# Kernel tuning notes

Hardware: AMD Instinct MI355X
Metric: run time of the kernel (lower is better)

## Reference

```python
import jax, jax.numpy as jnp
import numpy as np

GRID_SIZE = 5
SPLINE_ORDER = 3
NUM_BASIS = GRID_SIZE + SPLINE_ORDER  # 8

def _grid():
    # Extended knot vector over [-1, 1]: G + 2k + 1 knots
    h = 2.0 / GRID_SIZE
    return jnp.asarray(-1.0 + h * np.arange(-SPLINE_ORDER, GRID_SIZE + SPLINE_ORDER + 1), dtype=jnp.float32)

def _bspline_basis(x, grid, k):
    # x: [B, D] -> bases [B, D, G + k] via Cox-de Boor recursion
    xe = x[..., None]
    b = ((xe >= grid[:-1]) & (xe < grid[1:])).astype(x.dtype)
    for p in range(1, k + 1):
        left = (xe - grid[:-(p + 1)]) / (grid[p:-1] - grid[:-(p + 1)]) * b[..., :-1]
        right = (grid[p + 1:] - xe) / (grid[p + 1:] - grid[1:-p]) * b[..., 1:]
        b = left + right
    return b

def setup_inputs() -> dict:
    key = jax.random.key(0)
    ks = jax.random.split(key, 10)
    B, D, U = 2048, 1024, 1024
    L = 3  # number of KAN sub-layers
    s = 0.05
    return {
        "x": jax.random.normal(ks[0], (B, D), jnp.float32),
        "h_prev": jax.random.normal(ks[1], (B, U), jnp.float32),
        "c_prev": jax.random.normal(ks[2], (B, U), jnp.float32),
        "lstm_kernel": jax.random.normal(ks[3], (D, 4 * U), jnp.float32) * s,
        "lstm_rkernel": jax.random.normal(ks[4], (U, 4 * U), jnp.float32) * s,
        "lstm_bias": jnp.zeros((4 * U,), jnp.float32),
        "kan_base_w": jax.random.normal(ks[5], (L, D, U), jnp.float32) * s,
        "kan_spline_w": jax.random.normal(ks[6], (L, D * NUM_BASIS, U), jnp.float32) * s,
        "combine_w": jax.random.normal(ks[7], (U + L * U, U), jnp.float32) * s,
        "combine_b": jnp.zeros((U,), jnp.float32),
    }

def reference(x, h_prev, c_prev, lstm_kernel, lstm_rkernel, lstm_bias,
              kan_base_w, kan_spline_w, combine_w, combine_b):
    B, D = x.shape
    L, _, U = kan_base_w.shape
    # --- LSTM cell (Keras gate order i, f, g, o) ---
    z = x @ lstm_kernel + h_prev @ lstm_rkernel + lstm_bias
    zi, zf, zg, zo = jnp.split(z, 4, axis=-1)
    c = jax.nn.sigmoid(zf) * c_prev + jax.nn.sigmoid(zi) * jnp.tanh(zg)
    h = jax.nn.sigmoid(zo) * jnp.tanh(c)
    lstm_out = h
    # --- KAN sub-layers: silu(x) @ W_base + Bspline(x) @ W_spline ---
    grid = _grid()
    bases = _bspline_basis(x, grid, SPLINE_ORDER)           # [B, D, K]
    base_out = jnp.einsum('bd,ldu->lbu', jax.nn.silu(x), kan_base_w)
    spline_w = kan_spline_w.reshape(L, D, NUM_BASIS, U)
    spline_out = jnp.einsum('bdk,ldku->lbu', bases, spline_w)
    kan_out = base_out + spline_out                          # [L, B, U]
    kan_concat = jnp.transpose(kan_out, (1, 0, 2)).reshape(B, L * U)
    # --- fuse ---
    combined = jnp.concatenate([lstm_out, kan_concat], axis=-1)
    output = combined @ combine_w + combine_b
    return (output, h, c)
```

## Files before the change

kernel.cpp:

```cpp
#include <hip/hip_runtime.h>
#include <hip/hip_bf16.h>
#include <math.h>

#define B_SZ 2048
#define D_SZ 1024
#define U_SZ 1024
#define L_SZ 3
#define NB 8
#define KAN_K (D_SZ + D_SZ * NB)
#define KAN_N (L_SZ * U_SZ)
#define LSTM_K (D_SZ + U_SZ)
#define COMB_K (U_SZ + L_SZ * U_SZ)
#define LSTM_N (4 * U_SZ)

typedef __attribute__((ext_vector_type(8))) short bhalf8_t;
typedef __attribute__((ext_vector_type(4))) float floatx4_t;

__device__ inline void async_copy16(const void* g, void* l) {
  __builtin_amdgcn_global_load_lds(
      (const __attribute__((address_space(1))) void*)g,
      (__attribute__((address_space(3))) void*)l, 16, 0, 0);
}

__device__ inline float fsig(float v) { return 1.f / (1.f + __expf(-v)); }
__device__ inline float ftanh(float v) { return 1.f - 2.f / (__expf(2.f * v) + 1.f); }
__device__ inline unsigned short bfb(float v) {
  __hip_bfloat16 h = __float2bfloat16(v);
  return *(unsigned short*)&h;
}

__global__ __launch_bounds__(256) void prep_trans(
    const float* __restrict__ x, const float* __restrict__ h_prev,
    const float* __restrict__ lstm_k, const float* __restrict__ lstm_r,
    const float* __restrict__ comb_w, const float* __restrict__ base_w,
    const float* __restrict__ spline_w,
    __hip_bfloat16* __restrict__ A1, __hip_bfloat16* __restrict__ Akan,
    __hip_bfloat16* __restrict__ Bt1, __hip_bfloat16* __restrict__ Btc,
    __hip_bfloat16* __restrict__ Btk) {
  __shared__ float tile[64][65];
  int bid = blockIdx.x;
  int tid = threadIdx.x;
  if (bid < 8192) {
    int idx = bid * 256 + tid;
    int b = idx >> 10, d = idx & 1023;
    float xv = x[idx];
    float hv = h_prev[idx];
    A1[(size_t)b * LSTM_K + d] = __float2bfloat16(xv);
    A1[(size_t)b * LSTM_K + D_SZ + d] = __float2bfloat16(hv);
    float sg = 1.0f / (1.0f + __expf(-xv));
    Akan[(size_t)b * KAN_K + d] = __float2bfloat16(xv * sg);
    float t[12];
#pragma unroll
    for (int i = 0; i < 12; ++i) t[i] = (float)(-1.0 + 0.4 * (double)(i - 3));
    float bb[11];
#pragma unroll
    for (int j = 0; j < 11; ++j) bb[j] = (xv >= t[j] && xv < t[j + 1]) ? 1.0f : 0.0f;
#pragma unroll
    for (int p = 1; p <= 3; ++p) {
#pragma unroll
      for (int j = 0; j + p < 11; ++j) {
        float invl = 1.0f / (t[j + p] - t[j]);
        float invr = 1.0f / (t[j + p + 1] - t[j + 1]);
        bb[j] = (xv - t[j]) * invl * bb[j] + (t[j + p + 1] - xv) * invr * bb[j + 1];
      }
    }
    unsigned short o[8];
#pragma unroll
    for (int j = 0; j < 8; ++j) o[j] = bfb(bb[j]);
    *(uint4*)(Akan + (size_t)b * KAN_K + D_SZ + d * 8) = *(uint4*)o;
    return;
  }
  int id = bid - 8192;
  const float* src;
  __hip_bfloat16* dst;
  int srcLd, dstLd, gxs;
  if (id < 1024) {
    src = lstm_k; dst = Bt1; srcLd = 4096; dstLd = 2048; gxs = 6;
  } else if (id < 2048) {
    id -= 1024; src = lstm_r; dst = Bt1 + 1024; srcLd = 4096; dstLd = 2048; gxs = 6;
  } else if (id < 3072) {
    id -= 2048; src = comb_w; dst = Btc; srcLd = 1024; dstLd = 4096; gxs = 4;
  } else if (id < 3840) {
    id -= 3072; int l = id >> 8; id &= 255;
    src = base_w + (size_t)l * 1048576;
    dst = Btk + (size_t)l * U_SZ * KAN_K;
    srcLd = 1024; dstLd = KAN_K; gxs = 4;
  } else {
    id -= 3840; int l = id >> 11; id &= 2047;
    src = spline_w + (size_t)l * 8388608;
    dst = Btk + (size_t)l * U_SZ * KAN_K + D_SZ;
    srcLd = 1024; dstLd = KAN_K; gxs = 4;
  }
  int n0 = (id & ((1 << gxs) - 1)) * 64;
  int k0 = (id >> gxs) * 64;
  int c4 = (tid & 15) * 4;
  int r0 = tid >> 4;
#pragma unroll
  for (int i = 0; i < 4; ++i) {
    int r = r0 + i * 16;
    const float4 v = *(const float4*)(src + (size_t)(k0 + r) * srcLd + n0 + c4);
    tile[r][c4 + 0] = v.x;
    tile[r][c4 + 1] = v.y;
    tile[r][c4 + 2] = v.z;
    tile[r][c4 + 3] = v.w;
  }
  __syncthreads();
  int kg = (tid & 15) * 4;
  int nn = tid >> 4;
#pragma unroll
  for (int i = 0; i < 4; ++i) {
    int n = nn + i * 16;
    ushort4 w;
    w.x = bfb(tile[kg + 0][n]);
    w.y = bfb(tile[kg + 1][n]);
    w.z = bfb(tile[kg + 2][n]);
    w.w = bfb(tile[kg + 3][n]);
    *(ushort4*)(dst + (size_t)(n0 + n) * dstLd + k0 + kg) = w;
  }
}

__device__ __forceinline__ void gemm_core(
    const __hip_bfloat16* __restrict__ A, const __hip_bfloat16* __restrict__ Bt,
    int lda, float* __restrict__ C, int ldc, int m0, int n0, int kBeg, int kEnd) {
  __shared__ __align__(16) char lds[32768];
  char* ldsA = lds;
  char* ldsB = lds + 16384;
  int tid = threadIdx.x;
  int lane = tid & 63;
  int wave = tid >> 6;
  int wm = wave >> 1, wn = wave & 1;
  int q = lane >> 4, l16 = lane & 15;

  floatx4_t acc[4][4];
#pragma unroll
  for (int i = 0; i < 4; ++i)
#pragma unroll
    for (int j = 0; j < 4; ++j) acc[i][j] = (floatx4_t){0.f, 0.f, 0.f, 0.f};

  const __hip_bfloat16* Ab = A + (size_t)m0 * lda;
  const __hip_bfloat16* Bb = Bt + (size_t)n0 * lda;

  for (int k0 = kBeg; k0 < kEnd; k0 += 64) {
#pragma unroll
    for (int it = 0; it < 4; ++it) {
      int L = tid + it * 256;
      int n = L >> 3;
      int c = (L & 7) ^ (n & 7);
      async_copy16((const char*)(Ab + (size_t)n * lda + k0) + c * 16, ldsA + L * 16);
    }
#pragma unroll
    for (int it = 0; it < 4; ++it) {
      int L = tid + it * 256;
      int n = L >> 3;
      int c = (L & 7) ^ (n & 7);
      async_copy16((const char*)(Bb + (size_t)n * lda + k0) + c * 16, ldsB + L * 16);
    }
    __syncthreads();
#pragma unroll
    for (int s = 0; s < 2; ++s) {
      bhalf8_t af[4], bf[4];
#pragma unroll
      for (int mt = 0; mt < 4; ++mt) {
        int row = wm * 64 + mt * 16 + l16;
        int p = (s * 4 + q) ^ (row & 7);
        af[mt] = *(const bhalf8_t*)(ldsA + row * 128 + p * 16);
      }
#pragma unroll
      for (int nt = 0; nt < 4; ++nt) {
        int row = wn * 64 + nt * 16 + l16;
        int p = (s * 4 + q) ^ (row & 7);
        bf[nt] = *(const bhalf8_t*)(ldsB + row * 128 + p * 16);
      }
#pragma unroll
      for (int mt = 0; mt < 4; ++mt)
#pragma unroll
        for (int nt = 0; nt < 4; ++nt)
          acc[mt][nt] = __builtin_amdgcn_mfma_f32_16x16x32_bf16(af[mt], bf[nt], acc[mt][nt], 0, 0, 0);
    }
    __syncthreads();
  }
#pragma unroll
  for (int mt = 0; mt < 4; ++mt) {
#pragma unroll
    for (int nt = 0; nt < 4; ++nt) {
      int ccol = n0 + wn * 64 + nt * 16 + l16;
#pragma unroll
      for (int i = 0; i < 4; ++i) {
        int crow = m0 + wm * 64 + mt * 16 + q * 4 + i;
        C[(size_t)crow * ldc + ccol] = acc[mt][nt][i];
      }
    }
  }
}

__global__ __launch_bounds__(256) void gemm_multi(
    const __hip_bfloat16* __restrict__ A1, const __hip_bfloat16* __restrict__ Bt1,
    const __hip_bfloat16* __restrict__ Akan, const __hip_bfloat16* __restrict__ Btk,
    float* __restrict__ z, float* __restrict__ Pkan) {
  int id = blockIdx.x;
  if (id < 768) {
    int sk = id >= 384;
    int rem = id - sk * 384;
    int n0 = (rem % 24) * 128;
    int m0 = (rem / 24) * 128;
    gemm_core(Akan, Btk, KAN_K, Pkan + (size_t)sk * B_SZ * KAN_N, KAN_N,
              m0, n0, sk * 4608, (sk + 1) * 4608);
  } else {
    int j2 = id - 768;
    int n0 = (j2 & 31) * 128;
    int m0 = (j2 >> 5) * 128;
    gemm_core(A1, Bt1, LSTM_K, z, LSTM_N, m0, n0, 0, LSTM_K);
  }
}

__global__ __launch_bounds__(256) void reduce_fuse(
    const float* __restrict__ z, const float* __restrict__ c_prev,
    const float* __restrict__ bias, const float* __restrict__ Pkan,
    float* __restrict__ h_out, float* __restrict__ c_out,
    __hip_bfloat16* __restrict__ Acomb) {
  int bid = blockIdx.x;
  int tid = threadIdx.x;
  if (bid < 8192) {
    int idx = bid * 256 + tid;
    int b = idx >> 10, u = idx & 1023;
    const float* zr = z + (size_t)b * LSTM_N;
    float zi = zr[u] + bias[u];
    float zf = zr[U_SZ + u] + bias[U_SZ + u];
    float zg = zr[2 * U_SZ + u] + bias[2 * U_SZ + u];
    float zo = zr[3 * U_SZ + u] + bias[3 * U_SZ + u];
    float c = fsig(zf) * c_prev[idx] + fsig(zi) * ftanh(zg);
    float h = fsig(zo) * ftanh(c);
    h_out[idx] = h;
    c_out[idx] = c;
    Acomb[(size_t)b * COMB_K + u] = __float2bfloat16(h);
  } else {
    int g = (bid - 8192) * 256 + tid;
    int m = g / (KAN_N / 4);
    int c4 = (g - m * (KAN_N / 4)) * 4;
    const float4 p0 = *(const float4*)(Pkan + (size_t)m * KAN_N + c4);
    const float4 p1 = *(const float4*)(Pkan + (size_t)B_SZ * KAN_N + (size_t)m * KAN_N + c4);
    ushort4 o;
    o.x = bfb(p0.x + p1.x);
    o.y = bfb(p0.y + p1.y);
    o.z = bfb(p0.z + p1.z);
    o.w = bfb(p0.w + p1.w);
    *(ushort4*)(Acomb + (size_t)m * COMB_K + U_SZ + c4) = o;
  }
}

__global__ __launch_bounds__(256) void gemm_comb(
    const __hip_bfloat16* __restrict__ Acomb, const __hip_bfloat16* __restrict__ Btc,
    float* __restrict__ Pcomb) {
  int id = blockIdx.x;
  int sk = id >> 7;
  int rem = id & 127;
  int n0 = (rem & 7) * 128;
  int m0 = (rem >> 3) * 128;
  gemm_core(Acomb, Btc, COMB_K, Pcomb + (size_t)sk * B_SZ * U_SZ, U_SZ,
            m0, n0, sk * 1024, (sk + 1) * 1024);
}

__global__ __launch_bounds__(256) void comb_reduce(
    const float* __restrict__ Pcomb, const float* __restrict__ bias,
    float* __restrict__ out) {
  int g = blockIdx.x * 256 + threadIdx.x;
  int m = g >> 8;
  int c4 = (g & 255) * 4;
  float4 s = *(const float4*)(Pcomb + (size_t)m * U_SZ + c4);
  const size_t stride = (size_t)B_SZ * U_SZ;
#pragma unroll
  for (int p = 1; p < 4; ++p) {
    float4 t = *(const float4*)(Pcomb + stride * p + (size_t)m * U_SZ + c4);
    s.x += t.x; s.y += t.y; s.z += t.z; s.w += t.w;
  }
  float4 bv = *(const float4*)(bias + c4);
  s.x += bv.x; s.y += bv.y; s.z += bv.z; s.w += bv.w;
  *(float4*)(out + (size_t)m * U_SZ + c4) = s;
}

extern "C" void kernel_launch(void* const* d_in, const int* in_sizes, int n_in,
                              void* d_out, int out_size, void* d_ws, size_t ws_size,
                              hipStream_t stream) {
  const float* x        = (const float*)d_in[0];
  const float* h_prev   = (const float*)d_in[1];
  const float* c_prev   = (const float*)d_in[2];
  const float* lstm_k   = (const float*)d_in[3];
  const float* lstm_r   = (const float*)d_in[4];
  const float* lstm_b   = (const float*)d_in[5];
  const float* base_w   = (const float*)d_in[6];
  const float* spline_w = (const float*)d_in[7];
  const float* comb_w   = (const float*)d_in[8];
  const float* comb_b   = (const float*)d_in[9];
  float* out = (float*)d_out;

  char* ws = (char*)d_ws;
  auto alloc = [&](size_t bytes) {
    char* p = ws;
    ws += (bytes + 255) & ~(size_t)255;
    return p;
  };
  __hip_bfloat16* A1    = (__hip_bfloat16*)alloc((size_t)B_SZ * LSTM_K * 2);
  __hip_bfloat16* Akan  = (__hip_bfloat16*)alloc((size_t)B_SZ * KAN_K * 2);
  __hip_bfloat16* Acomb = (__hip_bfloat16*)alloc((size_t)B_SZ * COMB_K * 2);
  __hip_bfloat16* Bt1   = (__hip_bfloat16*)alloc((size_t)LSTM_N * LSTM_K * 2);
  __hip_bfloat16* Btk   = (__hip_bfloat16*)alloc((size_t)KAN_N * KAN_K * 2);
  __hip_bfloat16* Btc   = (__hip_bfloat16*)alloc((size_t)U_SZ * COMB_K * 2);
  float* z              = (float*)alloc((size_t)B_SZ * LSTM_N * 4);
  float* Pkan           = (float*)alloc((size_t)2 * B_SZ * KAN_N * 4);
  float* Pcomb          = Pkan;

  prep_trans<<<dim3(18176), 256, 0, stream>>>(x, h_prev, lstm_k, lstm_r, comb_w,
                                              base_w, spline_w, A1, Akan, Bt1, Btc, Btk);
  gemm_multi<<<dim3(1280), 256, 0, stream>>>(A1, Bt1, Akan, Btk, z, Pkan);
  reduce_fuse<<<dim3(14336), 256, 0, stream>>>(z, c_prev, lstm_b, Pkan,
                                               out + (size_t)B_SZ * U_SZ,
                                               out + 2 * (size_t)B_SZ * U_SZ, Acomb);
  gemm_comb<<<dim3(512), 256, 0, stream>>>(Acomb, Btc, Pcomb);
  comb_reduce<<<dim3(2048), 256, 0, stream>>>(Pcomb, comb_b, out);
}
```

Before: 510.1 us.

## Pre-multiply KAN weights with combine weights to shrink the activation GEMMs

Reassociates the KAN branch. On every call, the concatenated KAN base and spline weights are multiplied by the KAN slice of combine_w, giving a fused 9216x1024 bf16 weight, so activations go straight to U outputs instead of through a 3072-wide intermediate. The LSTM gate math and the KAN split-K GEMM now share one launch. A small final GEMM over h adds bias and the six split-K partials in its epilogue, replacing the separate reduce and combine kernels. This cuts total FLOPs and launches, at the cost of an extra bf16 rounding of the fused weight and larger fp32 partial buffers.

```diff
diff --git a/kernel.cpp b/kernel.cpp
--- a/kernel.cpp
+++ b/kernel.cpp
@@ -8,10 +8,10 @@
 #define L_SZ 3
 #define NB 8
 #define KAN_K (D_SZ + D_SZ * NB)
-#define KAN_N (L_SZ * U_SZ)
+#define WCAT_K (L_SZ * U_SZ)
 #define LSTM_K (D_SZ + U_SZ)
+#define LSTM_N (4 * U_SZ)
 #define COMB_K (U_SZ + L_SZ * U_SZ)
-#define LSTM_N (4 * U_SZ)
 
 typedef __attribute__((ext_vector_type(8))) short bhalf8_t;
 typedef __attribute__((ext_vector_type(4))) float floatx4_t;
@@ -27,6 +27,9 @@
 __device__ inline unsigned short bfb(float v) {
   __hip_bfloat16 h = __float2bfloat16(v);
   return *(unsigned short*)&h;
+}
+__device__ inline unsigned int bfb2(float lo, float hi) {
+  return (unsigned int)bfb(lo) | ((unsigned int)bfb(hi) << 16);
 }
 
 __global__ __launch_bounds__(256) void prep_trans(
@@ -36,7 +39,7 @@
     const float* __restrict__ spline_w,
     __hip_bfloat16* __restrict__ A1, __hip_bfloat16* __restrict__ Akan,
     __hip_bfloat16* __restrict__ Bt1, __hip_bfloat16* __restrict__ Btc,
-    __hip_bfloat16* __restrict__ Btk) {
+    __hip_bfloat16* __restrict__ Wcat) {
   __shared__ float tile[64][65];
   int bid = blockIdx.x;
   int tid = threadIdx.x;
@@ -70,6 +73,24 @@
     *(uint4*)(Akan + (size_t)b * KAN_K + D_SZ + d * 8) = *(uint4*)o;
     return;
   }
+  if (bid >= 11264) {
+    int e0 = (bid - 11264) * 2048 + tid * 8;
+    int kk = e0 / WCAT_K;
+    int col = e0 - kk * WCAT_K;
+    int l = col >> 10, u = col & 1023;
+    const float* srow = (kk < 1024)
+        ? base_w + ((size_t)l << 20) + (size_t)kk * 1024 + u
+        : spline_w + (size_t)l * 8388608 + (size_t)(kk - 1024) * 1024 + u;
+    float4 v0 = *(const float4*)(srow);
+    float4 v1 = *(const float4*)(srow + 4);
+    uint4 q;
+    q.x = bfb2(v0.x, v0.y);
+    q.y = bfb2(v0.z, v0.w);
+    q.z = bfb2(v1.x, v1.y);
+    q.w = bfb2(v1.z, v1.w);
+    *(uint4*)(Wcat + (size_t)kk * WCAT_K + col) = q;
+    return;
+  }
   int id = bid - 8192;
   const float* src;
   __hip_bfloat16* dst;
@@ -78,18 +99,8 @@
     src = lstm_k; dst = Bt1; srcLd = 4096; dstLd = 2048; gxs = 6;
   } else if (id < 2048) {
     id -= 1024; src = lstm_r; dst = Bt1 + 1024; srcLd = 4096; dstLd = 2048; gxs = 6;
-  } else if (id < 3072) {
+  } else {
     id -= 2048; src = comb_w; dst = Btc; srcLd = 1024; dstLd = 4096; gxs = 4;
-  } else if (id < 3840) {
-    id -= 3072; int l = id >> 8; id &= 255;
-    src = base_w + (size_t)l * 1048576;
-    dst = Btk + (size_t)l * U_SZ * KAN_K;
-    srcLd = 1024; dstLd = KAN_K; gxs = 4;
-  } else {
-    id -= 3840; int l = id >> 11; id &= 2047;
-    src = spline_w + (size_t)l * 8388608;
-    dst = Btk + (size_t)l * U_SZ * KAN_K + D_SZ;
-    srcLd = 1024; dstLd = KAN_K; gxs = 4;
   }
   int n0 = (id & ((1 << gxs) - 1)) * 64;
   int k0 = (id >> gxs) * 64;
@@ -119,9 +130,13 @@
   }
 }
 
+template <int EPI>
 __device__ __forceinline__ void gemm_core(
-    const __hip_bfloat16* __restrict__ A, const __hip_bfloat16* __restrict__ Bt,
-    int lda, float* __restrict__ C, int ldc, int m0, int n0, int kBeg, int kEnd) {
+    const __hip_bfloat16* __restrict__ A, int lda,
+    const __hip_bfloat16* __restrict__ Bt, int ldb,
+    void* __restrict__ Cout, int ldc, int m0, int n0, int kBeg, int kEnd,
+    const float* __restrict__ bias = nullptr,
+    const float* __restrict__ red = nullptr, size_t redStride = 0) {
   __shared__ __align__(16) char lds[32768];
   char* ldsA = lds;
   char* ldsB = lds + 16384;
@@ -138,7 +153,7 @@
     for (int j = 0; j < 4; ++j) acc[i][j] = (floatx4_t){0.f, 0.f, 0.f, 0.f};
 
   const __hip_bfloat16* Ab = A + (size_t)m0 * lda;
-  const __hip_bfloat16* Bb = Bt + (size_t)n0 * lda;
+  const __hip_bfloat16* Bb = Bt + (size_t)n0 * ldb;
 
   for (int k0 = kBeg; k0 < kEnd; k0 += 64) {
 #pragma unroll
@@ -153,7 +168,7 @@
       int L = tid + it * 256;
       int n = L >> 3;
       int c = (L & 7) ^ (n & 7);
-      async_copy16((const char*)(Bb + (size_t)n * lda + k0) + c * 16, ldsB + L * 16);
+      async_copy16((const char*)(Bb + (size_t)n * ldb + k0) + c * 16, ldsB + L * 16);
     }
     __syncthreads();
 #pragma unroll
@@ -187,7 +202,18 @@
 #pragma unroll
       for (int i = 0; i < 4; ++i) {
         int crow = m0 + wm * 64 + mt * 16 + q * 4 + i;
-        C[(size_t)crow * ldc + ccol] = acc[mt][nt][i];
+        float v = acc[mt][nt][i];
+        if (EPI == 0) {
+          ((float*)Cout)[(size_t)crow * ldc + ccol] = v;
+        } else if (EPI == 1) {
+          ((__hip_bfloat16*)Cout)[(size_t)crow * ldc + ccol] = __float2bfloat16(v);
+        } else {
+          v += bias[ccol];
+          size_t off = (size_t)crow * ldc + ccol;
+#pragma unroll
+          for (int p = 0; p < 6; ++p) v += red[redStride * p + off];
+          ((float*)Cout)[off] = v;
+        }
       }
     }
   }
@@ -195,87 +221,61 @@
 
 __global__ __launch_bounds__(256) void gemm_multi(
     const __hip_bfloat16* __restrict__ A1, const __hip_bfloat16* __restrict__ Bt1,
-    const __hip_bfloat16* __restrict__ Akan, const __hip_bfloat16* __restrict__ Btk,
-    float* __restrict__ z, float* __restrict__ Pkan) {
+    const __hip_bfloat16* __restrict__ Btc, const __hip_bfloat16* __restrict__ Wcat,
+    float* __restrict__ z, __hip_bfloat16* __restrict__ Wfsum) {
+  int id = blockIdx.x;
+  if (id < 576) {
+    int m0 = (id / 72) * 128;
+    int n0 = (id % 72) * 128;
+    gemm_core<1>(Btc + 1024, COMB_K, Wcat, WCAT_K, Wfsum, KAN_K,
+                 m0, n0, 0, WCAT_K);
+  } else {
+    int j2 = id - 576;
+    int n0 = (j2 & 31) * 128;
+    int m0 = (j2 >> 5) * 128;
+    gemm_core<0>(A1, LSTM_K, Bt1, LSTM_K, z, LSTM_N, m0, n0, 0, LSTM_K);
+  }
+}
+
+__global__ __launch_bounds__(256) void kan_gates(
+    const __hip_bfloat16* __restrict__ Akan, const __hip_bfloat16* __restrict__ Wfsum,
+    const float* __restrict__ z, const float* __restrict__ c_prev,
+    const float* __restrict__ bias, float* __restrict__ Pkan,
+    float* __restrict__ h_out, float* __restrict__ c_out,
+    __hip_bfloat16* __restrict__ Hb) {
   int id = blockIdx.x;
   if (id < 768) {
-    int sk = id >= 384;
-    int rem = id - sk * 384;
-    int n0 = (rem % 24) * 128;
-    int m0 = (rem / 24) * 128;
-    gemm_core(Akan, Btk, KAN_K, Pkan + (size_t)sk * B_SZ * KAN_N, KAN_N,
-              m0, n0, sk * 4608, (sk + 1) * 4608);
-  } else {
-    int j2 = id - 768;
-    int n0 = (j2 & 31) * 128;
-    int m0 = (j2 >> 5) * 128;
-    gemm_core(A1, Bt1, LSTM_K, z, LSTM_N, m0, n0, 0, LSTM_K);
-  }
-}
-
-__global__ __launch_bounds__(256) void reduce_fuse(
-    const float* __restrict__ z, const float* __restrict__ c_prev,
-    const float* __restrict__ bias, const float* __restrict__ Pkan,
-    float* __restrict__ h_out, float* __restrict__ c_out,
-    __hip_bfloat16* __restrict__ Acomb) {
-  int bid = blockIdx.x;
-  int tid = threadIdx.x;
-  if (bid < 8192) {
-    int idx = bid * 256 + tid;
-    int b = idx >> 10, u = idx & 1023;
-    const float* zr = z + (size_t)b * LSTM_N;
-    float zi = zr[u] + bias[u];
-    float zf = zr[U_SZ + u] + bias[U_SZ + u];
-    float zg = zr[2 * U_SZ + u] + bias[2 * U_SZ + u];
-    float zo = zr[3 * U_SZ + u] + bias[3 * U_SZ + u];
-    float c = fsig(zf) * c_prev[idx] + fsig(zi) * ftanh(zg);
-    float h = fsig(zo) * ftanh(c);
-    h_out[idx] = h;
-    c_out[idx] = c;
-    Acomb[(size_t)b * COMB_K + u] = __float2bfloat16(h);
-  } else {
-    int g = (bid - 8192) * 256 + tid;
-    int m = g / (KAN_N / 4);
-    int c4 = (g - m * (KAN_N / 4)) * 4;
-    const float4 p0 = *(const float4*)(Pkan + (size_t)m * KAN_N + c4);
-    const float4 p1 = *(const float4*)(Pkan + (size_t)B_SZ * KAN_N + (size_t)m * KAN_N + c4);
-    ushort4 o;
-    o.x = bfb(p0.x + p1.x);
-    o.y = bfb(p0.y + p1.y);
-    o.z = bfb(p0.z + p1.z);
-    o.w = bfb(p0.w + p1.w);
-    *(ushort4*)(Acomb + (size_t)m * COMB_K + U_SZ + c4) = o;
-  }
-}
-
-__global__ __launch_bounds__(256) void gemm_comb(
-    const __hip_bfloat16* __restrict__ Acomb, const __hip_bfloat16* __restrict__ Btc,
-    float* __restrict__ Pcomb) {
+    int sk = id >> 7;
+    int rem = id & 127;
+    int n0 = (rem & 7) * 128;
+    int m0 = (rem >> 3) * 128;
+    gemm_core<0>(Akan, KAN_K, Wfsum, KAN_K, Pkan + (size_t)sk * B_SZ * U_SZ, U_SZ,
+                 m0, n0, sk * 1536, sk * 1536 + 1536);
+    return;
+  }
+  int idx = (id - 768) * 256 + threadIdx.x;
+  int b = idx >> 10, u = idx & 1023;
+  const float* zr = z + (size_t)b * LSTM_N;
+  float zi = zr[u] + bias[u];
+  float zf = zr[U_SZ + u] + bias[U_SZ + u];
+  float zg = zr[2 * U_SZ + u] + bias[2 * U_SZ + u];
+  float zo = zr[3 * U_SZ + u] + bias[3 * U_SZ + u];
+  float c = fsig(zf) * c_prev[idx] + fsig(zi) * ftanh(zg);
+  float h = fsig(zo) * ftanh(c);
+  h_out[idx] = h;
+  c_out[idx] = c;
+  Hb[idx] = __float2bfloat16(h);
+}
+
+__global__ __launch_bounds__(256) void final_gemm(
+    const __hip_bfloat16* __restrict__ Hb, const __hip_bfloat16* __restrict__ Btc,
+    const float* __restrict__ Pkan, const float* __restrict__ comb_b,
+    float* __restrict__ out) {
   int id = blockIdx.x;
-  int sk = id >> 7;
-  int rem = id & 127;
-  int n0 = (rem & 7) * 128;
-  int m0 = (rem >> 3) * 128;
-  gemm_core(Acomb, Btc, COMB_K, Pcomb + (size_t)sk * B_SZ * U_SZ, U_SZ,
-            m0, n0, sk * 1024, (sk + 1) * 1024);
-}
-
-__global__ __launch_bounds__(256) void comb_reduce(
-    const float* __restrict__ Pcomb, const float* __restrict__ bias,
-    float* __restrict__ out) {
-  int g = blockIdx.x * 256 + threadIdx.x;
-  int m = g >> 8;
-  int c4 = (g & 255) * 4;
-  float4 s = *(const float4*)(Pcomb + (size_t)m * U_SZ + c4);
-  const size_t stride = (size_t)B_SZ * U_SZ;
-#pragma unroll
-  for (int p = 1; p < 4; ++p) {
-    float4 t = *(const float4*)(Pcomb + stride * p + (size_t)m * U_SZ + c4);
-    s.x += t.x; s.y += t.y; s.z += t.z; s.w += t.w;
-  }
-  float4 bv = *(const float4*)(bias + c4);
-  s.x += bv.x; s.y += bv.y; s.z += bv.z; s.w += bv.w;
-  *(float4*)(out + (size_t)m * U_SZ + c4) = s;
+  int n0 = (id & 7) * 128;
+  int m0 = (id >> 3) * 128;
+  gemm_core<3>(Hb, U_SZ, Btc, COMB_K, out, U_SZ, m0, n0, 0, U_SZ,
+               comb_b, Pkan, (size_t)B_SZ * U_SZ);
 }
 
 extern "C" void kernel_launch(void* const* d_in, const int* in_sizes, int n_in,
@@ -301,20 +301,19 @@
   };
   __hip_bfloat16* A1    = (__hip_bfloat16*)alloc((size_t)B_SZ * LSTM_K * 2);
   __hip_bfloat16* Akan  = (__hip_bfloat16*)alloc((size_t)B_SZ * KAN_K * 2);
-  __hip_bfloat16* Acomb = (__hip_bfloat16*)alloc((size_t)B_SZ * COMB_K * 2);
+  __hip_bfloat16* Hb    = (__hip_bfloat16*)alloc((size_t)B_SZ * U_SZ * 2);
   __hip_bfloat16* Bt1   = (__hip_bfloat16*)alloc((size_t)LSTM_N * LSTM_K * 2);
-  __hip_bfloat16* Btk   = (__hip_bfloat16*)alloc((size_t)KAN_N * KAN_K * 2);
   __hip_bfloat16* Btc   = (__hip_bfloat16*)alloc((size_t)U_SZ * COMB_K * 2);
+  __hip_bfloat16* Wcat  = (__hip_bfloat16*)alloc((size_t)KAN_K * WCAT_K * 2);
+  __hip_bfloat16* Wfsum = (__hip_bfloat16*)alloc((size_t)U_SZ * KAN_K * 2);
   float* z              = (float*)alloc((size_t)B_SZ * LSTM_N * 4);
-  float* Pkan           = (float*)alloc((size_t)2 * B_SZ * KAN_N * 4);
-  float* Pcomb          = Pkan;
-
-  prep_trans<<<dim3(18176), 256, 0, stream>>>(x, h_prev, lstm_k, lstm_r, comb_w,
-                                              base_w, spline_w, A1, Akan, Bt1, Btc, Btk);
-  gemm_multi<<<dim3(1280), 256, 0, stream>>>(A1, Bt1, Akan, Btk, z, Pkan);
-  reduce_fuse<<<dim3(14336), 256, 0, stream>>>(z, c_prev, lstm_b, Pkan,
-                                               out + (size_t)B_SZ * U_SZ,
-                                               out + 2 * (size_t)B_SZ * U_SZ, Acomb);
-  gemm_comb<<<dim3(512), 256, 0, stream>>>(Acomb, Btc, Pcomb);
-  comb_reduce<<<dim3(2048), 256, 0, stream>>>(Pcomb, comb_b, out);
-}
+  float* Pkan           = (float*)alloc((size_t)6 * B_SZ * U_SZ * 4);
+
+  prep_trans<<<dim3(25088), 256, 0, stream>>>(x, h_prev, lstm_k, lstm_r, comb_w,
+                                              base_w, spline_w, A1, Akan, Bt1, Btc, Wcat);
+  gemm_multi<<<dim3(1088), 256, 0, stream>>>(A1, Bt1, Btc, Wcat, z, Wfsum);
+  kan_gates<<<dim3(8960), 256, 0, stream>>>(Akan, Wfsum, z, c_prev, lstm_b, Pkan,
+                                            out + (size_t)B_SZ * U_SZ,
+                                            out + 2 * (size_t)B_SZ * U_SZ, Hb);
+  final_gemm<<<dim3(128), 256, 0, stream>>>(Hb, Btc, Pkan, comb_b, out);
+}
```

Result: faster. 495.2 us (-2.9%).
